# Kernel optimization log

Measured on AMD Instinct MI355X. Metric: run time of the kernel, lower is better.

The kernel has to match this reference:

```python
import jax, jax.numpy as jnp
import numpy as np

B, C_IN, C_OUT = 16, 64, 32
V_HI, V_LO, K = 163842, 40962, 7  # ico order-7 / order-6 vertex counts, 1-ring neighborhood size


def setup_inputs() -> dict:
    key = jax.random.key(0)
    k1, k2, k3, k4, k5 = jax.random.split(key, 5)
    x = jax.random.normal(k1, (B, C_IN, V_LO), dtype=jnp.float32)
    W = jax.random.normal(k2, (C_OUT, C_IN), dtype=jnp.float32) * 0.02
    b = jnp.zeros((C_OUT,), dtype=jnp.float32)
    max_pool_indices = jax.random.randint(k3, (B, C_OUT, V_LO), 0, K, dtype=jnp.int64 if jax.config.jax_enable_x64 else jnp.int32)
    up_neigh_indices = jax.random.randint(k4, (V_HI, K), 0, V_HI, dtype=jnp.int32)
    down_indices = jax.random.randint(k5, (V_LO,), 0, V_HI, dtype=jnp.int32)
    return {"x": x, "W": W, "b": b, "max_pool_indices": max_pool_indices,
            "up_neigh_indices": up_neigh_indices, "down_indices": down_indices}


def reference(x, W, b, max_pool_indices, up_neigh_indices, down_indices):
    # neigh_indices = up_neigh_indices[down_indices]  -> (V_LO, K)
    neigh_indices = up_neigh_indices[down_indices]
    n_samples, _, n_raw = x.shape
    # fc applied per-vertex on the feature axis: (B, C_IN, V) -> (B, C_OUT, V)
    h = jnp.einsum('bcv,oc->bov', x, W) + b[None, :, None]
    n_feats = W.shape[0]
    n_vertices = up_neigh_indices.shape[0]
    # vertices_indices[b, f, v] = neigh_indices[v, max_pool_indices[b, f, v]]
    vert_idx = neigh_indices[jnp.arange(n_raw)[None, None, :], max_pool_indices]  # (B, C_OUT, V_LO)
    # feats_indices exactly as original: floor(linspace(0, n_feats, n_raw*n_feats)), last -= 1
    feats_idx = np.floor(np.linspace(0.0, float(n_feats), num=n_raw * n_feats))
    feats_idx[-1] -= 1
    feats_idx = jnp.asarray(feats_idx.astype(np.int32))  # (C_OUT*V_LO,)
    h_flat = h.reshape(n_samples, -1)            # (B, C_OUT*V_LO), layout (feat, vertex)
    vert_flat = vert_idx.reshape(n_samples, -1)  # (B, C_OUT*V_LO)
    y = jnp.zeros((n_samples, n_feats, n_vertices), dtype=h.dtype)
    y = y.at[jnp.arange(n_samples)[:, None], feats_idx[None, :], vert_flat].set(h_flat)
    return y
```

## Files before the change

kernel.cpp:

```cpp
#include <hip/hip_runtime.h>
#include <hip/hip_bf16.h>
#include <stdint.h>

#define B_    16
#define C_IN  64
#define C_OUT 32
#define V_HI  163842
#define V_LO  40962
#define K_    7
#define TOTAL_E (V_LO * K_)
#define NPART 641

#define S_MP_BYTES 40968
#define GATHER_LDS (S_MP_BYTES + V_LO * 2 + 4)

__global__ __launch_bounds__(256) void compute_h_k(
    const float* __restrict__ x, const float* __restrict__ W,
    const float* __restrict__ bias, __hip_bfloat16* __restrict__ h)
{
    __shared__ float sW[C_OUT * C_IN];
    __shared__ float sB[C_OUT];
    int t = threadIdx.x;
    for (int i = t; i < C_OUT * C_IN; i += 256) sW[i] = W[i];
    if (t < C_OUT) sB[t] = bias[t];
    __syncthreads();

    int b = blockIdx.y;
    int v = blockIdx.x * 256 + t;
    if (v >= V_LO) return;

    const float* xp = x + (size_t)b * C_IN * V_LO + v;
    float acc[C_OUT];
#pragma unroll
    for (int o = 0; o < C_OUT; ++o) acc[o] = 0.0f;

    for (int c = 0; c < C_IN; ++c) {
        float xv = xp[(size_t)c * V_LO];
#pragma unroll
        for (int o = 0; o < C_OUT; ++o)
            acc[o] += xv * sW[o * C_IN + c];
    }

    __hip_bfloat16* hp = h + (size_t)b * C_OUT * V_LO + v;
#pragma unroll
    for (int o = 0; o < C_OUT; ++o)
        hp[(size_t)o * V_LO] = __float2bfloat16(acc[o] + sB[o]);
}

__global__ __launch_bounds__(256) void count_k(
    const int* __restrict__ up, const int* __restrict__ down,
    unsigned* __restrict__ cnt)
{
    int v = blockIdx.x * 256 + threadIdx.x;
    if (v >= V_LO) return;
    int d = down[v];
    const int* row = up + (size_t)d * K_;
    for (int k = 0; k < K_; ++k)
        atomicAdd(&cnt[row[k]], 1u);
}

__global__ __launch_bounds__(256) void blocksum_k(
    const unsigned* __restrict__ cnt, unsigned* __restrict__ partials)
{
    __shared__ unsigned s[256];
    int i = blockIdx.x * 256 + threadIdx.x;
    unsigned v = (i < V_HI) ? cnt[i] : 0u;
    s[threadIdx.x] = v;
    __syncthreads();
    for (int off = 128; off > 0; off >>= 1) {
        if (threadIdx.x < off) s[threadIdx.x] += s[threadIdx.x + off];
        __syncthreads();
    }
    if (threadIdx.x == 0) partials[blockIdx.x] = s[0];
}

__global__ __launch_bounds__(1024) void scanpart_k(unsigned* __restrict__ partials)
{
    __shared__ unsigned s[1024];
    int t = threadIdx.x;
    unsigned v = (t < NPART) ? partials[t] : 0u;
    s[t] = v;
    __syncthreads();
    for (int off = 1; off < 1024; off <<= 1) {
        unsigned add = (t >= off) ? s[t - off] : 0u;
        __syncthreads();
        s[t] += add;
        __syncthreads();
    }
    if (t < NPART) partials[t] = s[t] - v;
}

__global__ __launch_bounds__(256) void addoff_k(
    const unsigned* __restrict__ cnt, const unsigned* __restrict__ partials,
    unsigned* __restrict__ offsets, unsigned* __restrict__ cursor)
{
    __shared__ unsigned s[256];
    int t = threadIdx.x;
    int i = blockIdx.x * 256 + t;
    unsigned c = (i < V_HI) ? cnt[i] : 0u;
    s[t] = c;
    __syncthreads();
    for (int off = 1; off < 256; off <<= 1) {
        unsigned add = (t >= off) ? s[t - off] : 0u;
        __syncthreads();
        s[t] += add;
        __syncthreads();
    }
    unsigned excl = s[t] - c + partials[blockIdx.x];
    if (i < V_HI) { offsets[i] = excl; cursor[i] = excl; }
    if (i == 0) offsets[V_HI] = (unsigned)TOTAL_E;
}

__global__ __launch_bounds__(256) void scatter_k(
    const int* __restrict__ up, const int* __restrict__ down,
    unsigned* __restrict__ cursor, unsigned* __restrict__ entries)
{
    int v = blockIdx.x * 256 + threadIdx.x;
    if (v >= V_LO) return;
    int d = down[v];
    const int* row = up + (size_t)d * K_;
    for (int k = 0; k < K_; ++k) {
        int u = row[k];
        unsigned pos = atomicAdd(&cursor[u], 1u);
        entries[pos] = ((unsigned)v << 3) | (unsigned)k;
    }
}

__global__ __launch_bounds__(1024) void gather_out_k(
    const unsigned* __restrict__ offsets, const unsigned* __restrict__ entries,
    const int* __restrict__ mp, const ushort* __restrict__ h,
    float* __restrict__ out)
{
    extern __shared__ char smem[];
    unsigned char* s_mp = (unsigned char*)smem;
    ushort*        s_h  = (ushort*)(smem + S_MP_BYTES);

    int pair = blockIdx.x;
    const int*    mpp = mp  + (size_t)pair * V_LO;
    const ushort* hp  = h   + (size_t)pair * V_LO;
    float*        op  = out + (size_t)pair * V_HI;

    for (int i = threadIdx.x; i < V_LO; i += 1024) {
        s_mp[i] = (unsigned char)mpp[i];
        s_h[i]  = hp[i];
    }
    __syncthreads();

    for (int u = threadIdx.x; u < V_HI; u += 1024) {
        unsigned s0 = offsets[u];
        unsigned s1 = offsets[u + 1];
        int best = -1;
        for (unsigned e = s0; e < s1; ++e) {
            unsigned p = entries[e];
            int v = (int)(p >> 3);
            int k = (int)(p & 7u);
            if (s_mp[v] == (unsigned char)k && v > best) best = v;
        }
        float r = 0.0f;
        if (best >= 0)
            r = __uint_as_float(((unsigned)s_h[best]) << 16);
        op[u] = r;
    }
}

extern "C" void kernel_launch(void* const* d_in, const int* in_sizes, int n_in,
                              void* d_out, int out_size, void* d_ws, size_t ws_size,
                              hipStream_t stream)
{
    const float* x    = (const float*)d_in[0];
    const float* W    = (const float*)d_in[1];
    const float* bias = (const float*)d_in[2];
    const int*   mp   = (const int*)d_in[3];
    const int*   up   = (const int*)d_in[4];
    const int*   down = (const int*)d_in[5];
    float* out = (float*)d_out;

    char* ws = (char*)d_ws;
    const size_t H_BYTES   = (size_t)B_ * C_OUT * V_LO * sizeof(__hip_bfloat16);
    const size_t CNT_OFF   = H_BYTES;
    const size_t OFF_OFF   = CNT_OFF + (size_t)V_HI * 4;
    const size_t CUR_OFF   = OFF_OFF + (size_t)(V_HI + 1) * 4;
    const size_t ENT_OFF   = CUR_OFF + (size_t)V_HI * 4;
    const size_t PART_OFF  = ENT_OFF + (size_t)TOTAL_E * 4;

    __hip_bfloat16* h = (__hip_bfloat16*)ws;
    unsigned* cnt     = (unsigned*)(ws + CNT_OFF);
    unsigned* offsets = (unsigned*)(ws + OFF_OFF);
    unsigned* cursor  = (unsigned*)(ws + CUR_OFF);
    unsigned* entries = (unsigned*)(ws + ENT_OFF);
    unsigned* partials= (unsigned*)(ws + PART_OFF);

    (void)hipFuncSetAttribute((const void*)gather_out_k,
                              hipFuncAttributeMaxDynamicSharedMemorySize,
                              GATHER_LDS);

    hipMemsetAsync(cnt, 0, (size_t)V_HI * 4, stream);

    {
        dim3 grid((V_LO + 255) / 256, B_);
        compute_h_k<<<grid, 256, 0, stream>>>(x, W, bias, h);
    }

    {
        int vblk = (V_LO + 255) / 256;
        count_k<<<vblk, 256, 0, stream>>>(up, down, cnt);
        blocksum_k<<<NPART, 256, 0, stream>>>(cnt, partials);
        scanpart_k<<<1, 1024, 0, stream>>>(partials);
        addoff_k<<<NPART, 256, 0, stream>>>(cnt, partials, offsets, cursor);
        scatter_k<<<vblk, 256, 0, stream>>>(up, down, cursor, entries);
    }

    gather_out_k<<<B_ * C_OUT, 1024, GATHER_LDS, stream>>>(offsets, entries, mp, (const ushort*)h, out);
}
```

Baseline: 1.026 ms.

## Replace CSR gather with fused matmul and atomicMax scatter into output

```diff
diff --git a/kernel.cpp b/kernel.cpp
--- a/kernel.cpp
+++ b/kernel.cpp
@@ -8,26 +8,40 @@
 #define V_HI  163842
 #define V_LO  40962
 #define K_    7
-#define TOTAL_E (V_LO * K_)
-#define NPART 641
 
-#define S_MP_BYTES 40968
-#define GATHER_LDS (S_MP_BYTES + V_LO * 2 + 4)
+#define OUT_ELEMS ((size_t)B_ * C_OUT * V_HI)
+#define OUT_U4    (OUT_ELEMS / 4)
 
-__global__ __launch_bounds__(256) void compute_h_k(
+__global__ __launch_bounds__(256) void zero_k(uint4* __restrict__ p)
+{
+    size_t i = (size_t)blockIdx.x * 256 + threadIdx.x;
+    const size_t stride = (size_t)gridDim.x * 256;
+    const uint4 z = make_uint4(0u, 0u, 0u, 0u);
+    for (; i < OUT_U4; i += stride) p[i] = z;
+}
+
+__global__ __launch_bounds__(256) void fused_scatter_k(
     const float* __restrict__ x, const float* __restrict__ W,
-    const float* __restrict__ bias, __hip_bfloat16* __restrict__ h)
+    const float* __restrict__ bias, const int* __restrict__ mp,
+    const int* __restrict__ up, const int* __restrict__ down,
+    unsigned* __restrict__ out)
 {
     __shared__ float sW[C_OUT * C_IN];
     __shared__ float sB[C_OUT];
+    __shared__ int   sRow[K_ * 256];
     int t = threadIdx.x;
     for (int i = t; i < C_OUT * C_IN; i += 256) sW[i] = W[i];
     if (t < C_OUT) sB[t] = bias[t];
-    __syncthreads();
 
     int b = blockIdx.y;
     int v = blockIdx.x * 256 + t;
-    if (v >= V_LO) return;
+    bool valid = (v < V_LO);
+    int d = valid ? down[v] : 0;
+#pragma unroll
+    for (int k = 0; k < K_; ++k)
+        sRow[k * 256 + t] = valid ? up[(size_t)d * K_ + k] : 0;
+    __syncthreads();
+    if (!valid) return;
 
     const float* xp = x + (size_t)b * C_IN * V_LO + v;
     float acc[C_OUT];
@@ -41,125 +55,29 @@
             acc[o] += xv * sW[o * C_IN + c];
     }
 
-    __hip_bfloat16* hp = h + (size_t)b * C_OUT * V_LO + v;
+    const int* mpp = mp + (size_t)b * C_OUT * V_LO + v;
+    const unsigned vhi = (unsigned)v << 16;
 #pragma unroll
-    for (int o = 0; o < C_OUT; ++o)
-        hp[(size_t)o * V_LO] = __float2bfloat16(acc[o] + sB[o]);
-}
-
-__global__ __launch_bounds__(256) void count_k(
-    const int* __restrict__ up, const int* __restrict__ down,
-    unsigned* __restrict__ cnt)
-{
-    int v = blockIdx.x * 256 + threadIdx.x;
-    if (v >= V_LO) return;
-    int d = down[v];
-    const int* row = up + (size_t)d * K_;
-    for (int k = 0; k < K_; ++k)
-        atomicAdd(&cnt[row[k]], 1u);
-}
-
-__global__ __launch_bounds__(256) void blocksum_k(
-    const unsigned* __restrict__ cnt, unsigned* __restrict__ partials)
-{
-    __shared__ unsigned s[256];
-    int i = blockIdx.x * 256 + threadIdx.x;
-    unsigned v = (i < V_HI) ? cnt[i] : 0u;
-    s[threadIdx.x] = v;
-    __syncthreads();
-    for (int off = 128; off > 0; off >>= 1) {
-        if (threadIdx.x < off) s[threadIdx.x] += s[threadIdx.x + off];
-        __syncthreads();
-    }
-    if (threadIdx.x == 0) partials[blockIdx.x] = s[0];
-}
-
-__global__ __launch_bounds__(1024) void scanpart_k(unsigned* __restrict__ partials)
-{
-    __shared__ unsigned s[1024];
-    int t = threadIdx.x;
-    unsigned v = (t < NPART) ? partials[t] : 0u;
-    s[t] = v;
-    __syncthreads();
-    for (int off = 1; off < 1024; off <<= 1) {
-        unsigned add = (t >= off) ? s[t - off] : 0u;
-        __syncthreads();
-        s[t] += add;
-        __syncthreads();
-    }
-    if (t < NPART) partials[t] = s[t] - v;
-}
-
-__global__ __launch_bounds__(256) void addoff_k(
-    const unsigned* __restrict__ cnt, const unsigned* __restrict__ partials,
-    unsigned* __restrict__ offsets, unsigned* __restrict__ cursor)
-{
-    __shared__ unsigned s[256];
-    int t = threadIdx.x;
-    int i = blockIdx.x * 256 + t;
-    unsigned c = (i < V_HI) ? cnt[i] : 0u;
-    s[t] = c;
-    __syncthreads();
-    for (int off = 1; off < 256; off <<= 1) {
-        unsigned add = (t >= off) ? s[t - off] : 0u;
-        __syncthreads();
-        s[t] += add;
-        __syncthreads();
-    }
-    unsigned excl = s[t] - c + partials[blockIdx.x];
-    if (i < V_HI) { offsets[i] = excl; cursor[i] = excl; }
-    if (i == 0) offsets[V_HI] = (unsigned)TOTAL_E;
-}
-
-__global__ __launch_bounds__(256) void scatter_k(
-    const int* __restrict__ up, const int* __restrict__ down,
-    unsigned* __restrict__ cursor, unsigned* __restrict__ entries)
-{
-    int v = blockIdx.x * 256 + threadIdx.x;
-    if (v >= V_LO) return;
-    int d = down[v];
-    const int* row = up + (size_t)d * K_;
-    for (int k = 0; k < K_; ++k) {
-        int u = row[k];
-        unsigned pos = atomicAdd(&cursor[u], 1u);
-        entries[pos] = ((unsigned)v << 3) | (unsigned)k;
+    for (int o = 0; o < C_OUT; ++o) {
+        int k = mpp[(size_t)o * V_LO] & 7;
+        int u = sRow[k * 256 + t];
+        __hip_bfloat16 hv = __float2bfloat16(acc[o] + sB[o]);
+        unsigned hb = (unsigned)(*reinterpret_cast<unsigned short*>(&hv));
+        atomicMax(&out[((size_t)(b * C_OUT + o)) * V_HI + u], vhi | hb);
     }
 }
 
-__global__ __launch_bounds__(1024) void gather_out_k(
-    const unsigned* __restrict__ offsets, const unsigned* __restrict__ entries,
-    const int* __restrict__ mp, const ushort* __restrict__ h,
-    float* __restrict__ out)
+__global__ __launch_bounds__(256) void finalize_k(uint4* __restrict__ p)
 {
-    extern __shared__ char smem[];
-    unsigned char* s_mp = (unsigned char*)smem;
-    ushort*        s_h  = (ushort*)(smem + S_MP_BYTES);
-
-    int pair = blockIdx.x;
-    const int*    mpp = mp  + (size_t)pair * V_LO;
-    const ushort* hp  = h   + (size_t)pair * V_LO;
-    float*        op  = out + (size_t)pair * V_HI;
-
-    for (int i = threadIdx.x; i < V_LO; i += 1024) {
-        s_mp[i] = (unsigned char)mpp[i];
-        s_h[i]  = hp[i];
-    }
-    __syncthreads();
-
-    for (int u = threadIdx.x; u < V_HI; u += 1024) {
-        unsigned s0 = offsets[u];
-        unsigned s1 = offsets[u + 1];
-        int best = -1;
-        for (unsigned e = s0; e < s1; ++e) {
-            unsigned p = entries[e];
-            int v = (int)(p >> 3);
-            int k = (int)(p & 7u);
-            if (s_mp[v] == (unsigned char)k && v > best) best = v;
-        }
-        float r = 0.0f;
-        if (best >= 0)
-            r = __uint_as_float(((unsigned)s_h[best]) << 16);
-        op[u] = r;
+    size_t i = (size_t)blockIdx.x * 256 + threadIdx.x;
+    const size_t stride = (size_t)gridDim.x * 256;
+    for (; i < OUT_U4; i += stride) {
+        uint4 q = p[i];
+        q.x = (q.x & 0xFFFFu) << 16;
+        q.y = (q.y & 0xFFFFu) << 16;
+        q.z = (q.z & 0xFFFFu) << 16;
+        q.w = (q.w & 0xFFFFu) << 16;
+        p[i] = q;
     }
 }
 
@@ -173,42 +91,16 @@
     const int*   mp   = (const int*)d_in[3];
     const int*   up   = (const int*)d_in[4];
     const int*   down = (const int*)d_in[5];
-    float* out = (float*)d_out;
+    unsigned* outp = (unsigned*)d_out;
 
-    char* ws = (char*)d_ws;
-    const size_t H_BYTES   = (size_t)B_ * C_OUT * V_LO * sizeof(__hip_bfloat16);
-    const size_t CNT_OFF   = H_BYTES;
-    const size_t OFF_OFF   = CNT_OFF + (size_t)V_HI * 4;
-    const size_t CUR_OFF   = OFF_OFF + (size_t)(V_HI + 1) * 4;
-    const size_t ENT_OFF   = CUR_OFF + (size_t)V_HI * 4;
-    const size_t PART_OFF  = ENT_OFF + (size_t)TOTAL_E * 4;
+    (void)d_ws; (void)ws_size; (void)in_sizes; (void)n_in; (void)out_size;
 
-    __hip_bfloat16* h = (__hip_bfloat16*)ws;
-    unsigned* cnt     = (unsigned*)(ws + CNT_OFF);
-    unsigned* offsets = (unsigned*)(ws + OFF_OFF);
-    unsigned* cursor  = (unsigned*)(ws + CUR_OFF);
-    unsigned* entries = (unsigned*)(ws + ENT_OFF);
-    unsigned* partials= (unsigned*)(ws + PART_OFF);
-
-    (void)hipFuncSetAttribute((const void*)gather_out_k,
-                              hipFuncAttributeMaxDynamicSharedMemorySize,
-                              GATHER_LDS);
-
-    hipMemsetAsync(cnt, 0, (size_t)V_HI * 4, stream);
+    zero_k<<<8192, 256, 0, stream>>>((uint4*)outp);
 
     {
         dim3 grid((V_LO + 255) / 256, B_);
-        compute_h_k<<<grid, 256, 0, stream>>>(x, W, bias, h);
+        fused_scatter_k<<<grid, 256, 0, stream>>>(x, W, bias, mp, up, down, outp);
     }
 
-    {
-        int vblk = (V_LO + 255) / 256;
-        count_k<<<vblk, 256, 0, stream>>>(up, down, cnt);
-        blocksum_k<<<NPART, 256, 0, stream>>>(cnt, partials);
-        scanpart_k<<<1, 1024, 0, stream>>>(partials);
-        addoff_k<<<NPART, 256, 0, stream>>>(cnt, partials, offsets, cursor);
-        scatter_k<<<vblk, 256, 0, stream>>>(up, down, cursor, entries);
-    }
-
-    gather_out_k<<<B_ * C_OUT, 1024, GATHER_LDS, stream>>>(offsets, entries, mp, (const ushort*)h, out);
+    finalize_k<<<8192, 256, 0, stream>>>((uint4*)outp);
 }
```

Result: slower. 1.410 ms (+37.4%).
